# Performance work log

Measured on AMD Instinct MI355X. Metric: run time of the kernel, lower is better.

## Reference

```python
import jax, jax.numpy as jnp
import numpy as np
from jax import lax

D_MODEL = 128
D_INNER = 256      # expand=2 * d_model
D_STATE = 4
D_CONV = 4
DT_RANK = 16       # ceil(d_inner / 16), mamba-ssm default for the inner Mamba (expand=1)
DW_K = 3
B, H, W = 4, 64, 64


def setup_inputs() -> dict:
    key = jax.random.key(0)
    ks = jax.random.split(key, 16)
    g = lambda k, shape, s=0.02: jax.random.normal(k, shape, jnp.float32) * s
    inp = {}
    inp["x"] = jax.random.normal(ks[0], (B, D_MODEL, H, W), jnp.float32)
    inp["norm1_g"] = jnp.ones((D_MODEL,), jnp.float32)
    inp["norm1_b"] = jnp.zeros((D_MODEL,), jnp.float32)
    inp["in_proj_w"] = g(ks[1], (D_INNER, D_MODEL))
    inp["dwconv_w"] = g(ks[2], (D_INNER, 1, DW_K, DW_K), 0.1)
    # 4 independent Mamba modules (lr, rl, tb, bt), params stacked on axis 0
    inp["m_in_w"] = g(ks[3], (4, 2 * D_INNER, D_INNER))
    inp["m_conv_w"] = g(ks[4], (4, D_INNER, 1, D_CONV), 0.1)
    inp["m_conv_b"] = g(ks[5], (4, D_INNER), 0.1)
    inp["m_xproj_w"] = g(ks[6], (4, DT_RANK + 2 * D_STATE, D_INNER))
    inp["m_dt_w"] = g(ks[7], (4, D_INNER, DT_RANK), 0.1)
    inp["m_dt_b"] = jax.random.uniform(ks[8], (4, D_INNER), jnp.float32, -4.0, -2.0)
    inp["m_A_log"] = jnp.log(jnp.broadcast_to(
        jnp.arange(1, D_STATE + 1, dtype=jnp.float32), (4, D_INNER, D_STATE)))
    inp["m_D"] = jnp.ones((4, D_INNER), jnp.float32)
    inp["m_out_w"] = g(ks[9], (4, D_INNER, D_INNER))
    inp["normss_g"] = jnp.ones((D_INNER,), jnp.float32)
    inp["normss_b"] = jnp.zeros((D_INNER,), jnp.float32)
    inp["out_proj_w"] = g(ks[10], (D_MODEL, D_INNER))
    inp["norm2_g"] = jnp.ones((D_MODEL,), jnp.float32)
    inp["norm2_b"] = jnp.zeros((D_MODEL,), jnp.float32)
    inp["ffn_w1"] = g(ks[11], (D_MODEL, D_MODEL))
    inp["ffn_w2"] = g(ks[12], (D_MODEL, D_MODEL))
    return inp


def layer_norm(x, g, b, eps=1e-5):
    m = x.mean(-1, keepdims=True)
    v = ((x - m) ** 2).mean(-1, keepdims=True)
    return (x - m) * lax.rsqrt(v + eps) * g + b


def silu(x):
    return x * jax.nn.sigmoid(x)


def causal_dwconv1d(x, w, b):
    # x: (B, L, D); w: (D, 1, K) depthwise; left-pad K-1 (mamba pads both sides then truncates to L)
    xt = x.transpose(0, 2, 1)  # (B, D, L)
    y = lax.conv_general_dilated(xt, w, (1,), [(w.shape[-1] - 1, 0)],
                                 dimension_numbers=('NCH', 'OIH', 'NCH'),
                                 feature_group_count=xt.shape[1])
    return (y + b[None, :, None]).transpose(0, 2, 1)


def mamba(x, in_w, conv_w, conv_b, xproj_w, dt_w, dt_b, A_log, Dp, out_w):
    # x: (B, L, D) with D = D_INNER; inner Mamba has expand=1 so d_inner == d_model here
    Bb, L, Dm = x.shape
    xz = x @ in_w.T                                  # (B, L, 2D)
    xm, z = jnp.split(xz, 2, axis=-1)
    xm = silu(causal_dwconv1d(xm, conv_w, conv_b))   # (B, L, D)
    x_dbl = xm @ xproj_w.T                           # (B, L, dt_rank + 2N)
    dt = x_dbl[..., :DT_RANK]
    Bm = x_dbl[..., DT_RANK:DT_RANK + D_STATE]       # (B, L, N)
    Cm = x_dbl[..., DT_RANK + D_STATE:]              # (B, L, N)
    dt = jax.nn.softplus(dt @ dt_w.T + dt_b)         # (B, L, D)
    A = -jnp.exp(A_log)                              # (D, N)
    dA = jnp.exp(dt[..., None] * A)                  # (B, L, D, N)
    dBx = dt[..., None] * Bm[:, :, None, :] * xm[..., None]

    def step(h, inp):
        dA_t, dBx_t, C_t = inp
        h = dA_t * h + dBx_t                         # (B, D, N)
        return h, jnp.einsum('bdn,bn->bd', h, C_t)

    h0 = jnp.zeros((Bb, Dm, D_STATE), x.dtype)
    _, ys = lax.scan(step, h0, (dA.transpose(1, 0, 2, 3),
                                dBx.transpose(1, 0, 2, 3),
                                Cm.transpose(1, 0, 2)))
    y = ys.transpose(1, 0, 2) + Dp * xm              # (B, L, D)
    y = y * silu(z)
    return y @ out_w.T


def ss2d(h, Hh, Ww, mp):
    # h: (B, L, D). 4 directions: lr, rl (flip), tb (transpose), bt (transpose+flip)
    Bb, L, Dm = h.shape
    x_tb = h.reshape(Bb, Hh, Ww, Dm).transpose(0, 2, 1, 3).reshape(Bb, L, Dm)
    xs = jnp.stack([h, jnp.flip(h, 1), x_tb, jnp.flip(x_tb, 1)], 0)  # (4, B, L, D)
    ys = jax.vmap(mamba)(xs, *mp)                                     # (4, B, L, D)
    untb = lambda y: y.reshape(Bb, Ww, Hh, Dm).transpose(0, 2, 1, 3).reshape(Bb, L, Dm)
    y_lr = ys[0]
    y_rl = jnp.flip(ys[1], 1)
    y_tb = untb(ys[2])
    y_bt = untb(jnp.flip(ys[3], 1))
    return (y_lr + y_rl + y_tb + y_bt) / 4.0


def reference(x, norm1_g, norm1_b, in_proj_w, dwconv_w,
              m_in_w, m_conv_w, m_conv_b, m_xproj_w, m_dt_w, m_dt_b,
              m_A_log, m_D, m_out_w,
              normss_g, normss_b, out_proj_w,
              norm2_g, norm2_b, ffn_w1, ffn_w2):
    Bb, C, Hh, Ww = x.shape
    L = Hh * Ww
    x_flat = x.transpose(0, 2, 3, 1).reshape(Bb, L, C)
    x1 = layer_norm(x_flat, norm1_g, norm1_b)
    h = x1 @ in_proj_w.T                             # (B, L, d_inner)
    h2d = h.reshape(Bb, Hh, Ww, D_INNER).transpose(0, 3, 1, 2)
    p = DW_K // 2
    h2d = lax.conv_general_dilated(h2d, dwconv_w, (1, 1), [(p, p), (p, p)],
                                   dimension_numbers=('NCHW', 'OIHW', 'NCHW'),
                                   feature_group_count=D_INNER)
    h = silu(h2d.transpose(0, 2, 3, 1).reshape(Bb, L, D_INNER))
    mp = (m_in_w, m_conv_w, m_conv_b, m_xproj_w, m_dt_w, m_dt_b, m_A_log, m_D, m_out_w)
    h = ss2d(h, Hh, Ww, mp)
    h = layer_norm(h, normss_g, normss_b)
    h = h @ out_proj_w.T
    x2 = x_flat + h
    h2 = jax.nn.gelu(layer_norm(x2, norm2_g, norm2_b) @ ffn_w1.T, approximate=False) @ ffn_w2.T
    y = x2 + h2
    return y.reshape(Bb, Hh, Ww, C).transpose(0, 3, 1, 2)
```

## Files before the change

### kernel.cpp

```cpp
#include <hip/hip_runtime.h>
#include <math.h>


#define B_N   4
#define CDM   128
#define HH    64
#define WW    64
#define LL    4096
#define DI    256
#define DS    4
#define DCV   4
#define DTR   16
#define CS    32
#define NC    (LL / CS)
#define BLT   16384

typedef float    f32x4  __attribute__((ext_vector_type(4)));
typedef __bf16   bf16x8 __attribute__((ext_vector_type(8)));

__device__ __forceinline__ float silu_f(float x) { return x / (1.f + __expf(-x)); }
__device__ __forceinline__ float softplus_f(float x) {
  return fmaxf(x, 0.f) + __logf(1.f + __expf(-fabsf(x)));
}
__device__ __forceinline__ float gelu_f(float x) {
  return 0.5f * x * (1.f + erff(x * 0.70710678118654752f));
}
__device__ __forceinline__ ushort f2bf(float x) {
  unsigned u = __builtin_bit_cast(unsigned, x);
  u += 0x7fffu + ((u >> 16) & 1u);
  return (ushort)(u >> 16);
}
__device__ __forceinline__ float bf2f(ushort u) {
  return __builtin_bit_cast(float, (unsigned)u << 16);
}

__device__ __forceinline__ int sigma_map(int dir, int t) {
  int tt = (dir & 1) ? (LL - 1 - t) : t;
  if (dir >= 2) tt = ((tt & 63) << 6) | (tt >> 6);
  return tt;
}

#define GLDS(gp, lp) __builtin_amdgcn_global_load_lds( \
    (const __attribute__((address_space(1))) void*)(gp), \
    (__attribute__((address_space(3))) void*)(lp), 16, 0, 0)

__global__ void __launch_bounds__(256) k_prep(
    const float* __restrict__ s0, const float* __restrict__ s1,
    const float* __restrict__ s2, const float* __restrict__ s3,
    const float* __restrict__ s4, const float* __restrict__ s5,
    ushort* __restrict__ dst,
    const float* __restrict__ dtw, const float* __restrict__ xpw,
    ushort* __restrict__ w_dt, ushort* __restrict__ w_bc)
{
  int blk = blockIdx.x;
  if (blk < 864) {
    int i = (blk * 256 + threadIdx.x) * 4;
    const float* s; int base;
    if      (i < 32768)  { s = s0; base = 0; }
    else if (i < 557056) { s = s1; base = 32768; }
    else if (i < 819200) { s = s2; base = 557056; }
    else if (i < 851968) { s = s3; base = 819200; }
    else if (i < 868352) { s = s4; base = 851968; }
    else if (i < 884736) { s = s5; base = 868352; }
    else return;
    float4 v = *(const float4*)(s + (i - base));
    dst[i+0] = f2bf(v.x); dst[i+1] = f2bf(v.y); dst[i+2] = f2bf(v.z); dst[i+3] = f2bf(v.w);
  } else {
    int idx = (blk - 864) * 256 + threadIdx.x;
    if (idx >= 4 * 272 * 256) return;
    int dir = idx / 69632; int rem = idx - dir * 69632;
    int n = rem >> 8; int k = rem & 255;
    if (n < 256) {
      const float* dw = dtw + ((size_t)dir * DI + n) * DTR;
      const float* xp = xpw + (size_t)dir * 6144 + k;
      float acc = 0.f;
      #pragma unroll
      for (int j = 0; j < DTR; ++j) acc += dw[j] * xp[j * DI];
      w_dt[(size_t)dir * 65536 + (size_t)n * 256 + k] = f2bf(acc);
    } else {
      int n2 = n - 256;
      float v = (n2 < 8) ? xpw[(size_t)dir * 6144 + (size_t)(16 + n2) * 256 + k] : 0.f;
      w_bc[(size_t)dir * 4096 + (size_t)n2 * 256 + k] = f2bf(v);
    }
  }
}

__global__ void __launch_bounds__(256) k_ln1(
    const float* __restrict__ x, const float* __restrict__ g,
    const float* __restrict__ be, float* __restrict__ xflat,
    ushort* __restrict__ x1b)
{
  int blk = blockIdx.x;
  int b = blk >> 6; int l0 = (blk & 63) << 6;
  __shared__ float T[64][129];
  __shared__ float mrow[64], rrow[64];
  int t = threadIdx.x;
  int wv = t >> 6, lane = t & 63;
  for (int c = wv; c < CDM; c += 4)
    T[lane][c] = x[((size_t)b * CDM + c) * LL + l0 + lane];
  __syncthreads();
  int row = t >> 2, seg = t & 3;
  float s = 0.f;
  #pragma unroll
  for (int j = 0; j < 32; ++j) s += T[row][seg * 32 + j];
  s += __shfl_xor(s, 1); s += __shfl_xor(s, 2);
  float mean = s * (1.f / CDM);
  float v2 = 0.f;
  #pragma unroll
  for (int j = 0; j < 32; ++j) { float d = T[row][seg * 32 + j] - mean; v2 += d * d; }
  v2 += __shfl_xor(v2, 1); v2 += __shfl_xor(v2, 2);
  if (seg == 0) { mrow[row] = mean; rrow[row] = rsqrtf(v2 * (1.f / CDM) + 1e-5f); }
  __syncthreads();
  int c = t & 127;
  float gc = g[c], bc = be[c];
  for (int r = (t >> 7); r < 64; r += 2) {
    float v = T[r][c];
    size_t o = ((size_t)(b << 12) + l0 + r) * CDM + c;
    xflat[o] = v;
    x1b[o] = f2bf((v - mrow[r]) * rrow[r] * gc + bc);
  }
}

__global__ void __launch_bounds__(256) k_lnw256(
    const ushort* __restrict__ in, const float* __restrict__ g,
    const float* __restrict__ be, ushort* __restrict__ out)
{
  int w = threadIdx.x >> 6, lane = threadIdx.x & 63;
  int row = (blockIdx.x << 2) + w;
  size_t off = (size_t)row * DI + (lane << 2);
  ushort4 v4 = *(const ushort4*)(in + off);
  float v0 = bf2f(v4.x), v1 = bf2f(v4.y), v2 = bf2f(v4.z), v3 = bf2f(v4.w);
  float s1 = v0 + v1 + v2 + v3;
  float s2 = v0 * v0 + v1 * v1 + v2 * v2 + v3 * v3;
  #pragma unroll
  for (int o = 1; o < 64; o <<= 1) { s1 += __shfl_xor(s1, o); s2 += __shfl_xor(s2, o); }
  float mean = s1 * (1.f / DI);
  float r = rsqrtf(s2 * (1.f / DI) - mean * mean + 1e-5f);
  int c = lane << 2;
  ushort4 o4;
  o4.x = f2bf((v0 - mean) * r * g[c + 0] + be[c + 0]);
  o4.y = f2bf((v1 - mean) * r * g[c + 1] + be[c + 1]);
  o4.z = f2bf((v2 - mean) * r * g[c + 2] + be[c + 2]);
  o4.w = f2bf((v3 - mean) * r * g[c + 3] + be[c + 3]);
  *(ushort4*)(out + off) = o4;
}

template<int GATHER, int EPI, int BZ>
__global__ void __launch_bounds__(256) k_mgemm(
    const ushort* __restrict__ A, int lda,
    const ushort* __restrict__ Wt,
    float* __restrict__ Cf, ushort* __restrict__ Cb,
    int ldc, int K, const float* __restrict__ aux)
{
  if (BZ) {
    int z = blockIdx.z;
    A  += (size_t)z * BLT * DI;
    Wt += (size_t)z * DI * DI;
    if (Cb) Cb += (size_t)z * BLT * DI;
    if (aux) aux += (size_t)z * DI;
  }
  __shared__ ushort SH[16384];
  int tid = threadIdx.x;
  int m0 = blockIdx.x << 7, n0 = blockIdx.y << 7;
  int lane = tid & 63;
  int wm = ((tid >> 7) & 1) * 64;
  int wn = ((tid >> 6) & 1) * 64;
  int r15 = lane & 15, khi = lane >> 4;

  int srow = tid >> 3;
  int scol = (tid & 7) << 3;
  int arow[4], wrow[4];
  #pragma unroll
  for (int i = 0; i < 4; ++i) { arow[i] = m0 + i * 32 + srow; wrow[i] = n0 + i * 32 + srow; }

  f32x4 acc[4][4] = {};
  int wavebase = (tid & 192) * 8;

  for (int ks = 0; ks < K; ks += 64) {
    if (ks) __syncthreads();
    int dir = (GATHER == 2) ? (ks >> 8) : 0;
    int kin = (GATHER == 2) ? (ks & 255) : ks;
    #pragma unroll
    for (int i = 0; i < 4; ++i) {
      const ushort* gA = (GATHER == 2)
          ? A + (size_t)dir * (BLT * DI) + (size_t)arow[i] * DI + kin + scol
          : A + (size_t)arow[i] * lda + kin + scol;
      GLDS(gA, SH + i * 2048 + wavebase);
    }
    #pragma unroll
    for (int i = 0; i < 4; ++i) {
      const ushort* gW = (GATHER == 2)
          ? Wt + (size_t)dir * (DI * DI) + (size_t)wrow[i] * DI + kin + scol
          : Wt + (size_t)wrow[i] * K + kin + scol;
      GLDS(gW, SH + 8192 + i * 2048 + wavebase);
    }
    __syncthreads();
    #pragma unroll
    for (int kk = 0; kk < 2; ++kk) {
      bf16x8 af[4], wf[4];
      #pragma unroll
      for (int mi = 0; mi < 4; ++mi)
        af[mi] = *(const bf16x8*)&SH[(wm + mi * 16 + r15) * 64 + kk * 32 + khi * 8];
      #pragma unroll
      for (int ni = 0; ni < 4; ++ni)
        wf[ni] = *(const bf16x8*)&SH[8192 + (wn + ni * 16 + r15) * 64 + kk * 32 + khi * 8];
      #pragma unroll
      for (int mi = 0; mi < 4; ++mi)
        #pragma unroll
        for (int ni = 0; ni < 4; ++ni)
          acc[mi][ni] = __builtin_amdgcn_mfma_f32_16x16x32_bf16(
              af[mi], wf[ni], acc[mi][ni], 0, 0, 0);
    }
  }

  __syncthreads();
  #pragma unroll
  for (int mi = 0; mi < 4; ++mi)
    #pragma unroll
    for (int j = 0; j < 4; ++j) {
      int rr = wm + mi * 16 + khi * 4 + j;
      int sw = (rr & 7) << 3;
      #pragma unroll
      for (int ni = 0; ni < 4; ++ni) {
        int cc = wn + ni * 16 + r15;
        float v = acc[mi][ni][j];
        ushort bvv;
        if      (EPI == 8)  bvv = f2bf(0.25f * v);
        else if (EPI == 10) bvv = f2bf(softplus_f(v + aux[n0 + cc]));
        else                bvv = f2bf(v);
        SH[rr * 128 + (cc ^ sw)] = bvv;
      }
    }
  __syncthreads();
  #pragma unroll
  for (int i = 0; i < 8; ++i) {
    int rr = i * 16 + (tid >> 4);
    int cc = (tid & 15) << 3;
    uint4 v = *(const uint4*)&SH[rr * 128 + (cc ^ ((rr & 7) << 3))];
    *(uint4*)&Cb[(size_t)(m0 + rr) * ldc + n0 + cc] = v;
  }
}

__global__ void __launch_bounds__(256) k_oplna(
    const ushort* __restrict__ A,
    const ushort* __restrict__ Wt,
    const float* __restrict__ xflat,
    const float* __restrict__ g, const float* __restrict__ be,
    float* __restrict__ x2, ushort* __restrict__ x3b)
{
  __shared__ ushort As[64 * 64];
  __shared__ ushort Ws[128 * 64];
  __shared__ float redA[64][2], redB[64][2];
  int tid = threadIdx.x;
  int m0 = blockIdx.x << 6;
  int lane = tid & 63;
  int wm = ((tid >> 7) & 1) * 32;
  int wn = ((tid >> 6) & 1) * 64;
  int r15 = lane & 15, khi = lane >> 4;
  int srow = tid >> 3, scol = (tid & 7) << 3;

  f32x4 acc[2][4] = {};
  for (int ks = 0; ks < 256; ks += 64) {
    if (ks) __syncthreads();
    #pragma unroll
    for (int i = 0; i < 2; ++i) {
      const ushort* gA = A + (size_t)(m0 + i * 32 + srow) * DI + ks + scol;
      GLDS(gA, As + i * 2048 + tid * 8);
    }
    #pragma unroll
    for (int i = 0; i < 4; ++i) {
      const ushort* gW = Wt + (size_t)(i * 32 + srow) * DI + ks + scol;
      GLDS(gW, Ws + i * 2048 + tid * 8);
    }
    __syncthreads();
    #pragma unroll
    for (int kk = 0; kk < 2; ++kk) {
      bf16x8 af[2], wf[4];
      #pragma unroll
      for (int mi = 0; mi < 2; ++mi)
        af[mi] = *(const bf16x8*)&As[(wm + mi * 16 + r15) * 64 + kk * 32 + khi * 8];
      #pragma unroll
      for (int ni = 0; ni < 4; ++ni)
        wf[ni] = *(const bf16x8*)&Ws[(wn + ni * 16 + r15) * 64 + kk * 32 + khi * 8];
      #pragma unroll
      for (int mi = 0; mi < 2; ++mi)
        #pragma unroll
        for (int ni = 0; ni < 4; ++ni)
          acc[mi][ni] = __builtin_amdgcn_mfma_f32_16x16x32_bf16(
              af[mi], wf[ni], acc[mi][ni], 0, 0, 0);
    }
  }
  float vbuf[2][4][4];
  #pragma unroll
  for (int mi = 0; mi < 2; ++mi)
    #pragma unroll
    for (int j = 0; j < 4; ++j) {
      int rr = wm + mi * 16 + khi * 4 + j;
      float s1 = 0.f, s2 = 0.f;
      #pragma unroll
      for (int ni = 0; ni < 4; ++ni) {
        int cc = wn + ni * 16 + r15;
        float v = acc[mi][ni][j] + xflat[(size_t)(m0 + rr) * CDM + cc];
        vbuf[mi][ni][j] = v;
        s1 += v; s2 += v * v;
      }
      #pragma unroll
      for (int o = 1; o < 16; o <<= 1) { s1 += __shfl_xor(s1, o); s2 += __shfl_xor(s2, o); }
      if (r15 == 0) { redA[rr][wn >> 6] = s1; redB[rr][wn >> 6] = s2; }
    }
  __syncthreads();
  #pragma unroll
  for (int mi = 0; mi < 2; ++mi)
    #pragma unroll
    for (int j = 0; j < 4; ++j) {
      int rr = wm + mi * 16 + khi * 4 + j;
      float mean = (redA[rr][0] + redA[rr][1]) * (1.f / CDM);
      float var  = (redB[rr][0] + redB[rr][1]) * (1.f / CDM) - mean * mean;
      float rstd = rsqrtf(var + 1e-5f);
      #pragma unroll
      for (int ni = 0; ni < 4; ++ni) {
        int cc = wn + ni * 16 + r15;
        size_t off = (size_t)(m0 + rr) * CDM + cc;
        float v = vbuf[mi][ni][j];
        x2[off] = v;
        x3b[off] = f2bf((v - mean) * rstd * g[cc] + be[cc]);
      }
    }
}

__global__ void __launch_bounds__(256) k_ffn(
    const ushort* __restrict__ x3b, const ushort* __restrict__ w1,
    const ushort* __restrict__ w2, const float* __restrict__ x2,
    float* __restrict__ out)
{
  __shared__ ushort SH[20480];
  ushort* stageA = SH;
  ushort* stageW = SH + 4096;
  ushort* f1     = SH + 12288;
  float*  T      = (float*)SH;
  int tid = threadIdx.x;
  int m0 = blockIdx.x << 6;
  int b = m0 >> 12, l0 = m0 & (LL - 1);
  int lane = tid & 63;
  int wm = ((tid >> 7) & 1) * 32;
  int wn = ((tid >> 6) & 1) * 64;
  int r15 = lane & 15, khi = lane >> 4;
  int srow = tid >> 3, scol = (tid & 7) << 3;

  f32x4 acc[2][4] = {};
  for (int ks = 0; ks < 128; ks += 64) {
    if (ks) __syncthreads();
    #pragma unroll
    for (int i = 0; i < 2; ++i)
      GLDS(x3b + (size_t)(m0 + i * 32 + srow) * CDM + ks + scol, stageA + i * 2048 + tid * 8);
    #pragma unroll
    for (int i = 0; i < 4; ++i)
      GLDS(w1 + (size_t)(i * 32 + srow) * CDM + ks + scol, stageW + i * 2048 + tid * 8);
    __syncthreads();
    #pragma unroll
    for (int kk = 0; kk < 2; ++kk) {
      bf16x8 af[2], wf[4];
      #pragma unroll
      for (int mi = 0; mi < 2; ++mi)
        af[mi] = *(const bf16x8*)&stageA[(wm + mi * 16 + r15) * 64 + kk * 32 + khi * 8];
      #pragma unroll
      for (int ni = 0; ni < 4; ++ni)
        wf[ni] = *(const bf16x8*)&stageW[(wn + ni * 16 + r15) * 64 + kk * 32 + khi * 8];
      #pragma unroll
      for (int mi = 0; mi < 2; ++mi)
        #pragma unroll
        for (int ni = 0; ni < 4; ++ni)
          acc[mi][ni] = __builtin_amdgcn_mfma_f32_16x16x32_bf16(
              af[mi], wf[ni], acc[mi][ni], 0, 0, 0);
    }
  }
  __syncthreads();
  #pragma unroll
  for (int mi = 0; mi < 2; ++mi)
    #pragma unroll
    for (int j = 0; j < 4; ++j) {
      int rr = wm + mi * 16 + khi * 4 + j;
      int sw = (rr & 7) << 3;
      #pragma unroll
      for (int ni = 0; ni < 4; ++ni) {
        int cc = wn + ni * 16 + r15;
        f1[rr * 128 + (cc ^ sw)] = f2bf(gelu_f(acc[mi][ni][j]));
      }
    }
  __syncthreads();
  f32x4 acc2[2][4] = {};
  for (int ks = 0; ks < 128; ks += 64) {
    __syncthreads();
    #pragma unroll
    for (int i = 0; i < 4; ++i)
      GLDS(w2 + (size_t)(i * 32 + srow) * CDM + ks + scol, stageW + i * 2048 + tid * 8);
    __syncthreads();
    #pragma unroll
    for (int kk = 0; kk < 2; ++kk) {
      bf16x8 af[2], wf[4];
      #pragma unroll
      for (int mi = 0; mi < 2; ++mi) {
        int row = wm + mi * 16 + r15;
        int kx = (ks + kk * 32 + khi * 8) ^ ((row & 7) << 3);
        af[mi] = *(const bf16x8*)&f1[row * 128 + kx];
      }
      #pragma unroll
      for (int ni = 0; ni < 4; ++ni)
        wf[ni] = *(const bf16x8*)&stageW[(wn + ni * 16 + r15) * 64 + kk * 32 + khi * 8];
      #pragma unroll
      for (int mi = 0; mi < 2; ++mi)
        #pragma unroll
        for (int ni = 0; ni < 4; ++ni)
          acc2[mi][ni] = __builtin_amdgcn_mfma_f32_16x16x32_bf16(
              af[mi], wf[ni], acc2[mi][ni], 0, 0, 0);
    }
  }
  __syncthreads();
  #pragma unroll
  for (int mi = 0; mi < 2; ++mi)
    #pragma unroll
    for (int j = 0; j < 4; ++j) {
      int rr = wm + mi * 16 + khi * 4 + j;
      #pragma unroll
      for (int ni = 0; ni < 4; ++ni) {
        int cc = wn + ni * 16 + r15;
        T[rr * 129 + cc] = x2[(size_t)(m0 + rr) * CDM + cc] + acc2[mi][ni][j];
      }
    }
  __syncthreads();
  int q = tid >> 6;
  for (int cc = q; cc < CDM; cc += 4)
    out[(((size_t)b * CDM + cc) << 12) + l0 + lane] = T[lane * 129 + cc];
}

__global__ void __launch_bounds__(256) k_dwconv(
    const ushort* __restrict__ h, const float* __restrict__ wgt,
    ushort* __restrict__ out)
{
  int p = blockIdx.x;
  int b = p >> 12; int l = p & (LL - 1);
  int hy = l >> 6, wx = l & 63;
  int d = threadIdx.x;
  float acc = 0.f;
  #pragma unroll
  for (int di = -1; di <= 1; ++di) {
    int yy = hy + di; if (yy < 0 || yy >= HH) continue;
    #pragma unroll
    for (int dj = -1; dj <= 1; ++dj) {
      int xx = wx + dj; if (xx < 0 || xx >= WW) continue;
      acc += wgt[d * 9 + (di + 1) * 3 + (dj + 1)] *
             bf2f(h[(((size_t)b << 12) + (yy << 6) + xx) * DI + d]);
    }
  }
  out[(size_t)p * DI + d] = f2bf(silu_f(acc));
}

__global__ void __launch_bounds__(256) k_conv1d4(
    const ushort* __restrict__ xz_all, const float* __restrict__ cw,
    const float* __restrict__ cb, ushort* __restrict__ xmc4)
{
  int blk = blockIdx.x;
  int dir = blk >> 8; int b = (blk >> 6) & 3; int ch = blk & 63;
  int t0 = ch << 6;
  int d = threadIdx.x;
  const float* cwd = cw + (dir * DI + d) * DCV;
  float w0 = cwd[0], w1 = cwd[1], w2 = cwd[2], w3 = cwd[3];
  float bias = cb[dir * DI + d];
  size_t colb = (size_t)(dir << 9) + d;
  size_t rowb = (size_t)(b << 12);
  float xm3 = 0.f, xm2 = 0.f, xm1 = 0.f;
  if (t0 >= 3) {
    xm3 = bf2f(xz_all[(rowb + sigma_map(dir, t0 - 3)) * 2048 + colb]);
    xm2 = bf2f(xz_all[(rowb + sigma_map(dir, t0 - 2)) * 2048 + colb]);
    xm1 = bf2f(xz_all[(rowb + sigma_map(dir, t0 - 1)) * 2048 + colb]);
  }
  size_t obase = ((size_t)dir * BLT + (b << 12) + t0) * DI + d;
  #pragma unroll 4
  for (int i = 0; i < 64; ++i) {
    int l = sigma_map(dir, t0 + i);
    float x0 = bf2f(xz_all[(rowb + l) * 2048 + colb]);
    float acc = bias + w0 * xm3 + w1 * xm2 + w2 * xm1 + w3 * x0;
    xm3 = xm2; xm2 = xm1; xm1 = x0;
    xmc4[obase + (size_t)i * DI] = f2bf(silu_f(acc));
  }
}

__global__ void __launch_bounds__(256) k_bc(
    const ushort* __restrict__ xmc4, const ushort* __restrict__ w_bc,
    float* __restrict__ xbc4)
{
  __shared__ ushort As[128 * 64];
  __shared__ ushort Bs[16 * 64];
  int blk = blockIdx.x;
  int dir = blk >> 7; int m0 = (blk & 127) << 7;
  int tid = threadIdx.x;
  int lane = tid & 63; int wv = tid >> 6;
  int r15 = lane & 15, khi = lane >> 4;
  int srow = tid >> 3, scol = (tid & 7) << 3;
  size_t abase = (size_t)dir * BLT * DI;
  f32x4 acc[2] = {};
  for (int ks = 0; ks < 256; ks += 64) {
    if (ks) __syncthreads();
    #pragma unroll
    for (int i = 0; i < 4; ++i) {
      const ushort* g = xmc4 + abase + (size_t)(m0 + i * 32 + srow) * DI + ks + scol;
      GLDS(g, As + i * 2048 + tid * 8);
    }
    if (tid < 128) {
      const ushort* g = w_bc + (size_t)dir * 4096 + (size_t)(tid >> 3) * 256 + ks + scol;
      GLDS(g, Bs + tid * 8);
    }
    __syncthreads();
    #pragma unroll
    for (int kk = 0; kk < 2; ++kk) {
      bf16x8 af0 = *(const bf16x8*)&As[((wv << 5) + r15) * 64 + kk * 32 + khi * 8];
      bf16x8 af1 = *(const bf16x8*)&As[((wv << 5) + 16 + r15) * 64 + kk * 32 + khi * 8];
      bf16x8 wf  = *(const bf16x8*)&Bs[r15 * 64 + kk * 32 + khi * 8];
      acc[0] = __builtin_amdgcn_mfma_f32_16x16x32_bf16(af0, wf, acc[0], 0, 0, 0);
      acc[1] = __builtin_amdgcn_mfma_f32_16x16x32_bf16(af1, wf, acc[1], 0, 0, 0);
    }
  }
  if (r15 < 8) {
    #pragma unroll
    for (int mi = 0; mi < 2; ++mi)
      #pragma unroll
      for (int j = 0; j < 4; ++j) {
        int row = m0 + (wv << 5) + mi * 16 + khi * 4 + j;
        xbc4[((size_t)dir * BLT + row) * 8 + r15] = acc[mi][j];
      }
  }
}

__global__ void __launch_bounds__(256) k_scan_part(
    const ushort* __restrict__ dt4, const ushort* __restrict__ xmc4,
    const float* __restrict__ xbc4, const float* __restrict__ Alog4,
    float* __restrict__ P4, float* __restrict__ H4)
{
  int blk = blockIdx.x;
  int dir = blk >> 9; int b = (blk >> 7) & 3; int ch = blk & (NC - 1);
  int d = threadIdx.x;
  const float* Alog = Alog4 + (size_t)dir * DI * DS;
  float Av[DS], h[DS], P[DS];
  #pragma unroll
  for (int n = 0; n < DS; ++n) { Av[n] = -__expf(Alog[d * DS + n]); h[n] = 0.f; P[n] = 1.f; }
  size_t seg = (size_t)dir * BLT;
  size_t base = seg + (size_t)b * LL + (size_t)ch * CS;
  #pragma unroll 4
  for (int t = 0; t < CS; ++t) {
    size_t r = base + t;
    float dt = bf2f(dt4[r * DI + d]);
    float xm = bf2f(xmc4[r * DI + d]);
    float4 Bv = *(const float4*)(xbc4 + r * 8);
    float bx = dt * xm;
    float dA0 = __expf(dt * Av[0]), dA1 = __expf(dt * Av[1]);
    float dA2 = __expf(dt * Av[2]), dA3 = __expf(dt * Av[3]);
    h[0] = dA0 * h[0] + bx * Bv.x; P[0] *= dA0;
    h[1] = dA1 * h[1] + bx * Bv.y; P[1] *= dA1;
    h[2] = dA2 * h[2] + bx * Bv.z; P[2] *= dA2;
    h[3] = dA3 * h[3] + bx * Bv.w; P[3] *= dA3;
  }
  size_t o = ((size_t)blk * DI + d) * DS;
  #pragma unroll
  for (int n = 0; n < DS; ++n) { P4[o + n] = P[n]; H4[o + n] = h[n]; }
}

__global__ void __launch_bounds__(256) k_scan_carry(
    const float* __restrict__ P4, float* __restrict__ H4)
{
  int idx = blockIdx.x * 256 + threadIdx.x;
  int dir = idx >> 12; int r = idx & 4095;
  int b = r >> 10; int dn = r & 1023;
  size_t sbase = ((size_t)dir * 512 + (size_t)b * NC) * 1024 + dn;
  float carry = 0.f;
  #pragma unroll 8
  for (int ch = 0; ch < NC; ++ch) {
    size_t o = sbase + (size_t)ch * 1024;
    float Pv = P4[o], Hv = H4[o];
    H4[o] = carry;
    carry = Pv * carry + Hv;
  }
}

__global__ void __launch_bounds__(256) k_scan_fix(
    const ushort* __restrict__ dt4, const ushort* __restrict__ xmc4,
    const float* __restrict__ xbc4, const ushort* __restrict__ xz_all,
    const float* __restrict__ Alog4, const float* __restrict__ Dp4,
    const float* __restrict__ Cin, ushort* __restrict__ ybuf4)
{
  int blk = blockIdx.x;
  int dir = blk >> 9; int b = (blk >> 7) & 3; int ch = blk & (NC - 1);
  int d = threadIdx.x;
  const float* Alog = Alog4 + (size_t)dir * DI * DS;
  float Av[DS], h[DS];
  size_t ci = ((size_t)blk * DI + d) * DS;
  #pragma unroll
  for (int n = 0; n < DS; ++n) { Av[n] = -__expf(Alog[d * DS + n]); h[n] = Cin[ci + n]; }
  float Dv = Dp4[dir * DI + d];
  size_t seg = (size_t)dir * BLT;
  size_t base = seg + (size_t)b * LL + (size_t)ch * CS;
  #pragma unroll 4
  for (int t = 0; t < CS; ++t) {
    size_t r = base + t;
    float dt = bf2f(dt4[r * DI + d]);
    float xm = bf2f(xmc4[r * DI + d]);
    float4 Bv = *(const float4*)(xbc4 + r * 8);
    float4 Cv = *(const float4*)(xbc4 + r * 8 + 4);
    float bx = dt * xm;
    float dA0 = __expf(dt * Av[0]), dA1 = __expf(dt * Av[1]);
    float dA2 = __expf(dt * Av[2]), dA3 = __expf(dt * Av[3]);
    h[0] = dA0 * h[0] + bx * Bv.x;
    h[1] = dA1 * h[1] + bx * Bv.y;
    h[2] = dA2 * h[2] + bx * Bv.z;
    h[3] = dA3 * h[3] + bx * Bv.w;
    float y = h[0] * Cv.x + h[1] * Cv.y + h[2] * Cv.z + h[3] * Cv.w;
    int l = sigma_map(dir, (ch << 5) + t);
    float zv = bf2f(xz_all[(((size_t)(b << 12)) + l) * 2048 + (dir << 9) + 256 + d]);
    ybuf4[(seg + (size_t)(b << 12) + l) * DI + d] = f2bf((y + Dv * xm) * silu_f(zv));
  }
}

extern "C" void kernel_launch(void* const* d_in, const int* in_sizes, int n_in,
                              void* d_out, int out_size, void* d_ws, size_t ws_size,
                              hipStream_t stream) {
  const float* x          = (const float*)d_in[0];
  const float* norm1_g    = (const float*)d_in[1];
  const float* norm1_b    = (const float*)d_in[2];
  const float* in_proj_w  = (const float*)d_in[3];
  const float* dwconv_w   = (const float*)d_in[4];
  const float* m_in_w     = (const float*)d_in[5];
  const float* m_conv_w   = (const float*)d_in[6];
  const float* m_conv_b   = (const float*)d_in[7];
  const float* m_xproj_w  = (const float*)d_in[8];
  const float* m_dt_w     = (const float*)d_in[9];
  const float* m_dt_b     = (const float*)d_in[10];
  const float* m_A_log    = (const float*)d_in[11];
  const float* m_D        = (const float*)d_in[12];
  const float* m_out_w    = (const float*)d_in[13];
  const float* normss_g   = (const float*)d_in[14];
  const float* normss_b   = (const float*)d_in[15];
  const float* out_proj_w = (const float*)d_in[16];
  const float* norm2_g    = (const float*)d_in[17];
  const float* norm2_b    = (const float*)d_in[18];
  const float* ffn_w1     = (const float*)d_in[19];
  const float* ffn_w2     = (const float*)d_in[20];

  float* ws = (float*)d_ws;
  size_t o = 0;
  auto alloc = [&](size_t nf) { float* p = ws + o; o += nf; return p; };
  const size_t BL = BLT;
  float* xflat = alloc(BL * CDM);
  float* x2    = alloc(BL * CDM);
  float* xbc4  = alloc(BL * 8 * 4);
  float* P4    = alloc((size_t)4 * B_N * NC * DI * DS);
  float* H4    = alloc((size_t)4 * B_N * NC * DI * DS);
  auto ualloc = [&](size_t nu) { ushort* p = (ushort*)(ws + o); o += (nu + 1) / 2; return p; };
  ushort* x1b    = ualloc(BL * CDM);
  ushort* hinb   = ualloc(BL * DI);
  ushort* hcb    = ualloc(BL * DI);
  ushort* xz_all = ualloc(BL * 2048);
  ushort* xmc4   = ualloc(BL * DI * 4);
  ushort* dt4    = ualloc(BL * DI * 4);
  ushort* ybuf4  = ualloc(BL * DI * 4);
  ushort* ycombb = ualloc(BL * DI);
  ushort* hlnb   = ualloc(BL * DI);
  ushort* x3b    = ualloc(BL * CDM);
  ushort* wb     = ualloc(884736);
  ushort* w_dt   = ualloc((size_t)4 * DI * DI);
  ushort* w_bc   = ualloc((size_t)4 * 16 * DI);
  ushort* w_inproj = wb + 0;
  ushort* w_min    = wb + 32768;
  ushort* w_mout   = wb + 557056;
  ushort* w_oproj  = wb + 819200;
  ushort* w_ffn1   = wb + 851968;
  ushort* w_ffn2   = wb + 868352;

  k_prep<<<1952, 256, 0, stream>>>(
      in_proj_w, m_in_w, m_out_w, out_proj_w, ffn_w1, ffn_w2, wb,
      m_dt_w, m_xproj_w, w_dt, w_bc);
  k_ln1<<<B_N * 64, 256, 0, stream>>>(x, norm1_g, norm1_b, xflat, x1b);
  k_mgemm<0, 6, 0><<<dim3(128, 2), 256, 0, stream>>>(
      x1b, CDM, w_inproj, nullptr, hinb, DI, CDM, nullptr);
  k_dwconv<<<B_N * LL, DI, 0, stream>>>(hinb, dwconv_w, hcb);
  k_mgemm<0, 6, 0><<<dim3(128, 16), 256, 0, stream>>>(
      hcb, DI, w_min, nullptr, xz_all, 2048, DI, nullptr);
  k_conv1d4<<<1024, 256, 0, stream>>>(xz_all, m_conv_w, m_conv_b, xmc4);
  k_mgemm<0, 10, 1><<<dim3(128, 2, 4), 256, 0, stream>>>(
      xmc4, DI, w_dt, nullptr, dt4, DI, DI, m_dt_b);
  k_bc<<<512, 256, 0, stream>>>(xmc4, w_bc, xbc4);
  k_scan_part<<<4 * B_N * NC, 256, 0, stream>>>(dt4, xmc4, xbc4, m_A_log, P4, H4);
  k_scan_carry<<<64, 256, 0, stream>>>(P4, H4);
  k_scan_fix<<<4 * B_N * NC, 256, 0, stream>>>(
      dt4, xmc4, xbc4, xz_all, m_A_log, m_D, H4, ybuf4);
  k_mgemm<2, 8, 0><<<dim3(128, 2), 256, 0, stream>>>(
      ybuf4, DI, w_mout, nullptr, ycombb, DI, 1024, nullptr);
  k_lnw256<<<BLT / 4, 256, 0, stream>>>(ycombb, normss_g, normss_b, hlnb);
  k_oplna<<<256, 256, 0, stream>>>(
      hlnb, w_oproj, xflat, norm2_g, norm2_b, x2, x3b);
  k_ffn<<<256, 256, 0, stream>>>(x3b, w_ffn1, w_ffn2, x2, (float*)d_out);
}
```

Before: 249.4 us.

## Fuse dt projection with chunk scan and fold SS2D LayerNorm into out-proj

The dt projection GEMM (softplus epilogue) is merged with the per-chunk partial scan, so each block computes dt for a 128-row tile and immediately scans its 32-step chunks from shared memory. The separate partial-scan kernel and the standalone LayerNorm kernel are removed, and the LayerNorm is applied inside the out-projection kernel on a fully staged 64x256 A tile. The residual input is now stored as bf16 instead of fp32 to cut bandwidth. This saves launches and global round trips, at the cost of lower residual precision and fewer threads running the scan (each thread does 2 chunks serially), which may reduce scan parallelism.

```diff
diff --git a/kernel.cpp b/kernel.cpp
--- a/kernel.cpp
+++ b/kernel.cpp
@@ -17,6 +17,7 @@
 
 typedef float    f32x4  __attribute__((ext_vector_type(4)));
 typedef __bf16   bf16x8 __attribute__((ext_vector_type(8)));
+typedef unsigned short u16x8 __attribute__((ext_vector_type(8)));
 
 __device__ __forceinline__ float silu_f(float x) { return x / (1.f + __expf(-x)); }
 __device__ __forceinline__ float softplus_f(float x) {
@@ -87,7 +88,7 @@
 
 __global__ void __launch_bounds__(256) k_ln1(
     const float* __restrict__ x, const float* __restrict__ g,
-    const float* __restrict__ be, float* __restrict__ xflat,
+    const float* __restrict__ be, ushort* __restrict__ xflatb,
     ushort* __restrict__ x1b)
 {
   int blk = blockIdx.x;
@@ -116,49 +117,17 @@
   for (int r = (t >> 7); r < 64; r += 2) {
     float v = T[r][c];
     size_t o = ((size_t)(b << 12) + l0 + r) * CDM + c;
-    xflat[o] = v;
+    xflatb[o] = f2bf(v);
     x1b[o] = f2bf((v - mrow[r]) * rrow[r] * gc + bc);
   }
 }
 
-__global__ void __launch_bounds__(256) k_lnw256(
-    const ushort* __restrict__ in, const float* __restrict__ g,
-    const float* __restrict__ be, ushort* __restrict__ out)
-{
-  int w = threadIdx.x >> 6, lane = threadIdx.x & 63;
-  int row = (blockIdx.x << 2) + w;
-  size_t off = (size_t)row * DI + (lane << 2);
-  ushort4 v4 = *(const ushort4*)(in + off);
-  float v0 = bf2f(v4.x), v1 = bf2f(v4.y), v2 = bf2f(v4.z), v3 = bf2f(v4.w);
-  float s1 = v0 + v1 + v2 + v3;
-  float s2 = v0 * v0 + v1 * v1 + v2 * v2 + v3 * v3;
-  #pragma unroll
-  for (int o = 1; o < 64; o <<= 1) { s1 += __shfl_xor(s1, o); s2 += __shfl_xor(s2, o); }
-  float mean = s1 * (1.f / DI);
-  float r = rsqrtf(s2 * (1.f / DI) - mean * mean + 1e-5f);
-  int c = lane << 2;
-  ushort4 o4;
-  o4.x = f2bf((v0 - mean) * r * g[c + 0] + be[c + 0]);
-  o4.y = f2bf((v1 - mean) * r * g[c + 1] + be[c + 1]);
-  o4.z = f2bf((v2 - mean) * r * g[c + 2] + be[c + 2]);
-  o4.w = f2bf((v3 - mean) * r * g[c + 3] + be[c + 3]);
-  *(ushort4*)(out + off) = o4;
-}
-
-template<int GATHER, int EPI, int BZ>
+template<int GATHER, int EPI>
 __global__ void __launch_bounds__(256) k_mgemm(
     const ushort* __restrict__ A, int lda,
     const ushort* __restrict__ Wt,
-    float* __restrict__ Cf, ushort* __restrict__ Cb,
-    int ldc, int K, const float* __restrict__ aux)
-{
-  if (BZ) {
-    int z = blockIdx.z;
-    A  += (size_t)z * BLT * DI;
-    Wt += (size_t)z * DI * DI;
-    if (Cb) Cb += (size_t)z * BLT * DI;
-    if (aux) aux += (size_t)z * DI;
-  }
+    ushort* __restrict__ Cb, int ldc, int K)
+{
   __shared__ ushort SH[16384];
   int tid = threadIdx.x;
   int m0 = blockIdx.x << 7, n0 = blockIdx.y << 7;
@@ -224,11 +193,7 @@
       for (int ni = 0; ni < 4; ++ni) {
         int cc = wn + ni * 16 + r15;
         float v = acc[mi][ni][j];
-        ushort bvv;
-        if      (EPI == 8)  bvv = f2bf(0.25f * v);
-        else if (EPI == 10) bvv = f2bf(softplus_f(v + aux[n0 + cc]));
-        else                bvv = f2bf(v);
-        SH[rr * 128 + (cc ^ sw)] = bvv;
+        SH[rr * 128 + (cc ^ sw)] = (EPI == 8) ? f2bf(0.25f * v) : f2bf(v);
       }
     }
   __syncthreads();
@@ -241,14 +206,118 @@
   }
 }
 
+__global__ void __launch_bounds__(256) k_dtscan(
+    const ushort* __restrict__ xmc4, const ushort* __restrict__ w_dt,
+    const float* __restrict__ dtb4, const float* __restrict__ xbc4,
+    const float* __restrict__ Alog4,
+    ushort* __restrict__ dt4, float* __restrict__ P4, float* __restrict__ H4)
+{
+  int z = blockIdx.z;
+  const ushort* A  = xmc4 + (size_t)z * BLT * DI;
+  const ushort* Wt = w_dt + (size_t)z * DI * DI;
+  ushort* Cb = dt4 + (size_t)z * BLT * DI;
+  const float* aux = dtb4 + z * DI;
+  __shared__ ushort SH[16384];
+  int tid = threadIdx.x;
+  int m0 = blockIdx.x << 7, n0 = blockIdx.y << 7;
+  int lane = tid & 63;
+  int wm = ((tid >> 7) & 1) * 64;
+  int wn = ((tid >> 6) & 1) * 64;
+  int r15 = lane & 15, khi = lane >> 4;
+  int srow = tid >> 3, scol = (tid & 7) << 3;
+
+  f32x4 acc[4][4] = {};
+  int wavebase = (tid & 192) * 8;
+  for (int ks = 0; ks < 256; ks += 64) {
+    if (ks) __syncthreads();
+    #pragma unroll
+    for (int i = 0; i < 4; ++i)
+      GLDS(A + (size_t)(m0 + i * 32 + srow) * DI + ks + scol, SH + i * 2048 + wavebase);
+    #pragma unroll
+    for (int i = 0; i < 4; ++i)
+      GLDS(Wt + (size_t)(n0 + i * 32 + srow) * DI + ks + scol, SH + 8192 + i * 2048 + wavebase);
+    __syncthreads();
+    #pragma unroll
+    for (int kk = 0; kk < 2; ++kk) {
+      bf16x8 af[4], wf[4];
+      #pragma unroll
+      for (int mi = 0; mi < 4; ++mi)
+        af[mi] = *(const bf16x8*)&SH[(wm + mi * 16 + r15) * 64 + kk * 32 + khi * 8];
+      #pragma unroll
+      for (int ni = 0; ni < 4; ++ni)
+        wf[ni] = *(const bf16x8*)&SH[8192 + (wn + ni * 16 + r15) * 64 + kk * 32 + khi * 8];
+      #pragma unroll
+      for (int mi = 0; mi < 4; ++mi)
+        #pragma unroll
+        for (int ni = 0; ni < 4; ++ni)
+          acc[mi][ni] = __builtin_amdgcn_mfma_f32_16x16x32_bf16(
+              af[mi], wf[ni], acc[mi][ni], 0, 0, 0);
+    }
+  }
+  __syncthreads();
+  #pragma unroll
+  for (int mi = 0; mi < 4; ++mi)
+    #pragma unroll
+    for (int j = 0; j < 4; ++j) {
+      int rr = wm + mi * 16 + khi * 4 + j;
+      int sw = (rr & 7) << 3;
+      #pragma unroll
+      for (int ni = 0; ni < 4; ++ni) {
+        int cc = wn + ni * 16 + r15;
+        SH[rr * 128 + (cc ^ sw)] = f2bf(softplus_f(acc[mi][ni][j] + aux[n0 + cc]));
+      }
+    }
+  __syncthreads();
+  #pragma unroll
+  for (int i = 0; i < 8; ++i) {
+    int rr = i * 16 + (tid >> 4);
+    int cc = (tid & 15) << 3;
+    uint4 v = *(const uint4*)&SH[rr * 128 + (cc ^ ((rr & 7) << 3))];
+    *(uint4*)&Cb[(size_t)(m0 + rr) * DI + n0 + cc] = v;
+  }
+  int dl = tid & 127;
+  int dg = n0 + dl;
+  const float* Alog = Alog4 + ((size_t)z * DI + dg) * DS;
+  float Av[DS];
+  #pragma unroll
+  for (int n = 0; n < DS; ++n) Av[n] = -__expf(Alog[n]);
+  #pragma unroll
+  for (int cc2 = 0; cc2 < 2; ++cc2) {
+    int chl = ((tid >> 7) << 1) + cc2;
+    float h0 = 0.f, h1 = 0.f, h2 = 0.f, h3 = 0.f;
+    float P0 = 1.f, P1 = 1.f, P2 = 1.f, P3 = 1.f;
+    #pragma unroll 4
+    for (int tl = 0; tl < CS; ++tl) {
+      int tr = (chl << 5) + tl;
+      float dt = bf2f(SH[tr * 128 + (dl ^ ((tr & 7) << 3))]);
+      float xm = bf2f(A[(size_t)(m0 + tr) * DI + dg]);
+      float4 Bv = *(const float4*)(xbc4 + ((size_t)z * BLT + m0 + tr) * 8);
+      float bx = dt * xm;
+      float dA0 = __expf(dt * Av[0]), dA1 = __expf(dt * Av[1]);
+      float dA2 = __expf(dt * Av[2]), dA3 = __expf(dt * Av[3]);
+      h0 = dA0 * h0 + bx * Bv.x; P0 *= dA0;
+      h1 = dA1 * h1 + bx * Bv.y; P1 *= dA1;
+      h2 = dA2 * h2 + bx * Bv.z; P2 *= dA2;
+      h3 = dA3 * h3 + bx * Bv.w; P3 *= dA3;
+    }
+    int b = (m0 + (chl << 5)) >> 12;
+    int ch_in_b = ((m0 & 4095) >> 5) + chl;
+    int blk = z * 512 + b * 128 + ch_in_b;
+    size_t o = ((size_t)blk * DI + dg) * DS;
+    *(float4*)(P4 + o) = make_float4(P0, P1, P2, P3);
+    *(float4*)(H4 + o) = make_float4(h0, h1, h2, h3);
+  }
+}
+
 __global__ void __launch_bounds__(256) k_oplna(
-    const ushort* __restrict__ A,
+    const ushort* __restrict__ yc,
     const ushort* __restrict__ Wt,
-    const float* __restrict__ xflat,
-    const float* __restrict__ g, const float* __restrict__ be,
+    const ushort* __restrict__ xflatb,
+    const float* __restrict__ gss, const float* __restrict__ bss,
+    const float* __restrict__ g2, const float* __restrict__ b2,
     float* __restrict__ x2, ushort* __restrict__ x3b)
 {
-  __shared__ ushort As[64 * 64];
+  __shared__ ushort Ash[64 * 256];
   __shared__ ushort Ws[128 * 64];
   __shared__ float redA[64][2], redB[64][2];
   int tid = threadIdx.x;
@@ -259,26 +328,53 @@
   int r15 = lane & 15, khi = lane >> 4;
   int srow = tid >> 3, scol = (tid & 7) << 3;
 
+  #pragma unroll
+  for (int i = 0; i < 8; ++i)
+    GLDS(yc + (size_t)m0 * DI + i * 2048 + tid * 8, Ash + i * 2048 + tid * 8);
+  __syncthreads();
+  {
+    int r = tid >> 2, q = tid & 3;
+    float vreg[8][8];
+    float s1 = 0.f, s2 = 0.f;
+    #pragma unroll
+    for (int j = 0; j < 8; ++j) {
+      int ch = (j + tid) & 7;
+      u16x8 v8 = *(const u16x8*)&Ash[r * 256 + q * 64 + ch * 8];
+      #pragma unroll
+      for (int e = 0; e < 8; ++e) {
+        float v = bf2f(v8[e]);
+        vreg[j][e] = v; s1 += v; s2 += v * v;
+      }
+    }
+    s1 += __shfl_xor(s1, 1); s1 += __shfl_xor(s1, 2);
+    s2 += __shfl_xor(s2, 1); s2 += __shfl_xor(s2, 2);
+    float mean = s1 * (1.f / DI);
+    float rstd = rsqrtf(s2 * (1.f / DI) - mean * mean + 1e-5f);
+    #pragma unroll
+    for (int j = 0; j < 8; ++j) {
+      int ch = (j + tid) & 7;
+      int colb = q * 64 + ch * 8;
+      u16x8 o8;
+      #pragma unroll
+      for (int e = 0; e < 8; ++e)
+        o8[e] = f2bf((vreg[j][e] - mean) * rstd * gss[colb + e] + bss[colb + e]);
+      *(u16x8*)&Ash[r * 256 + colb] = o8;
+    }
+  }
+  __syncthreads();
   f32x4 acc[2][4] = {};
   for (int ks = 0; ks < 256; ks += 64) {
     if (ks) __syncthreads();
     #pragma unroll
-    for (int i = 0; i < 2; ++i) {
-      const ushort* gA = A + (size_t)(m0 + i * 32 + srow) * DI + ks + scol;
-      GLDS(gA, As + i * 2048 + tid * 8);
-    }
-    #pragma unroll
-    for (int i = 0; i < 4; ++i) {
-      const ushort* gW = Wt + (size_t)(i * 32 + srow) * DI + ks + scol;
-      GLDS(gW, Ws + i * 2048 + tid * 8);
-    }
+    for (int i = 0; i < 4; ++i)
+      GLDS(Wt + (size_t)(i * 32 + srow) * DI + ks + scol, Ws + i * 2048 + tid * 8);
     __syncthreads();
     #pragma unroll
     for (int kk = 0; kk < 2; ++kk) {
       bf16x8 af[2], wf[4];
       #pragma unroll
       for (int mi = 0; mi < 2; ++mi)
-        af[mi] = *(const bf16x8*)&As[(wm + mi * 16 + r15) * 64 + kk * 32 + khi * 8];
+        af[mi] = *(const bf16x8*)&Ash[(wm + mi * 16 + r15) * 256 + ks + kk * 32 + khi * 8];
       #pragma unroll
       for (int ni = 0; ni < 4; ++ni)
         wf[ni] = *(const bf16x8*)&Ws[(wn + ni * 16 + r15) * 64 + kk * 32 + khi * 8];
@@ -300,7 +396,7 @@
       #pragma unroll
       for (int ni = 0; ni < 4; ++ni) {
         int cc = wn + ni * 16 + r15;
-        float v = acc[mi][ni][j] + xflat[(size_t)(m0 + rr) * CDM + cc];
+        float v = acc[mi][ni][j] + bf2f(xflatb[(size_t)(m0 + rr) * CDM + cc]);
         vbuf[mi][ni][j] = v;
         s1 += v; s2 += v * v;
       }
@@ -323,7 +419,7 @@
         size_t off = (size_t)(m0 + rr) * CDM + cc;
         float v = vbuf[mi][ni][j];
         x2[off] = v;
-        x3b[off] = f2bf((v - mean) * rstd * g[cc] + be[cc]);
+        x3b[off] = f2bf((v - mean) * rstd * g2[cc] + b2[cc]);
       }
     }
 }
@@ -529,39 +625,6 @@
         xbc4[((size_t)dir * BLT + row) * 8 + r15] = acc[mi][j];
       }
   }
-}
-
-__global__ void __launch_bounds__(256) k_scan_part(
-    const ushort* __restrict__ dt4, const ushort* __restrict__ xmc4,
-    const float* __restrict__ xbc4, const float* __restrict__ Alog4,
-    float* __restrict__ P4, float* __restrict__ H4)
-{
-  int blk = blockIdx.x;
-  int dir = blk >> 9; int b = (blk >> 7) & 3; int ch = blk & (NC - 1);
-  int d = threadIdx.x;
-  const float* Alog = Alog4 + (size_t)dir * DI * DS;
-  float Av[DS], h[DS], P[DS];
-  #pragma unroll
-  for (int n = 0; n < DS; ++n) { Av[n] = -__expf(Alog[d * DS + n]); h[n] = 0.f; P[n] = 1.f; }
-  size_t seg = (size_t)dir * BLT;
-  size_t base = seg + (size_t)b * LL + (size_t)ch * CS;
-  #pragma unroll 4
-  for (int t = 0; t < CS; ++t) {
-    size_t r = base + t;
-    float dt = bf2f(dt4[r * DI + d]);
-    float xm = bf2f(xmc4[r * DI + d]);
-    float4 Bv = *(const float4*)(xbc4 + r * 8);
-    float bx = dt * xm;
-    float dA0 = __expf(dt * Av[0]), dA1 = __expf(dt * Av[1]);
-    float dA2 = __expf(dt * Av[2]), dA3 = __expf(dt * Av[3]);
-    h[0] = dA0 * h[0] + bx * Bv.x; P[0] *= dA0;
-    h[1] = dA1 * h[1] + bx * Bv.y; P[1] *= dA1;
-    h[2] = dA2 * h[2] + bx * Bv.z; P[2] *= dA2;
-    h[3] = dA3 * h[3] + bx * Bv.w; P[3] *= dA3;
-  }
-  size_t o = ((size_t)blk * DI + d) * DS;
-  #pragma unroll
-  for (int n = 0; n < DS; ++n) { P4[o + n] = P[n]; H4[o + n] = h[n]; }
 }
 
 __global__ void __launch_bounds__(256) k_scan_carry(
@@ -648,12 +711,12 @@
   size_t o = 0;
   auto alloc = [&](size_t nf) { float* p = ws + o; o += nf; return p; };
   const size_t BL = BLT;
-  float* xflat = alloc(BL * CDM);
   float* x2    = alloc(BL * CDM);
   float* xbc4  = alloc(BL * 8 * 4);
   float* P4    = alloc((size_t)4 * B_N * NC * DI * DS);
   float* H4    = alloc((size_t)4 * B_N * NC * DI * DS);
   auto ualloc = [&](size_t nu) { ushort* p = (ushort*)(ws + o); o += (nu + 1) / 2; return p; };
+  ushort* xflatb = ualloc(BL * CDM);
   ushort* x1b    = ualloc(BL * CDM);
   ushort* hinb   = ualloc(BL * DI);
   ushort* hcb    = ualloc(BL * DI);
@@ -662,7 +725,6 @@
   ushort* dt4    = ualloc(BL * DI * 4);
   ushort* ybuf4  = ualloc(BL * DI * 4);
   ushort* ycombb = ualloc(BL * DI);
-  ushort* hlnb   = ualloc(BL * DI);
   ushort* x3b    = ualloc(BL * CDM);
   ushort* wb     = ualloc(884736);
   ushort* w_dt   = ualloc((size_t)4 * DI * DI);
@@ -677,24 +739,22 @@
   k_prep<<<1952, 256, 0, stream>>>(
       in_proj_w, m_in_w, m_out_w, out_proj_w, ffn_w1, ffn_w2, wb,
       m_dt_w, m_xproj_w, w_dt, w_bc);
-  k_ln1<<<B_N * 64, 256, 0, stream>>>(x, norm1_g, norm1_b, xflat, x1b);
-  k_mgemm<0, 6, 0><<<dim3(128, 2), 256, 0, stream>>>(
-      x1b, CDM, w_inproj, nullptr, hinb, DI, CDM, nullptr);
+  k_ln1<<<B_N * 64, 256, 0, stream>>>(x, norm1_g, norm1_b, xflatb, x1b);
+  k_mgemm<0, 6><<<dim3(128, 2), 256, 0, stream>>>(
+      x1b, CDM, w_inproj, hinb, DI, CDM);
   k_dwconv<<<B_N * LL, DI, 0, stream>>>(hinb, dwconv_w, hcb);
-  k_mgemm<0, 6, 0><<<dim3(128, 16), 256, 0, stream>>>(
-      hcb, DI, w_min, nullptr, xz_all, 2048, DI, nullptr);
+  k_mgemm<0, 6><<<dim3(128, 16), 256, 0, stream>>>(
+      hcb, DI, w_min, xz_all, 2048, DI);
   k_conv1d4<<<1024, 256, 0, stream>>>(xz_all, m_conv_w, m_conv_b, xmc4);
-  k_mgemm<0, 10, 1><<<dim3(128, 2, 4), 256, 0, stream>>>(
-      xmc4, DI, w_dt, nullptr, dt4, DI, DI, m_dt_b);
   k_bc<<<512, 256, 0, stream>>>(xmc4, w_bc, xbc4);
-  k_scan_part<<<4 * B_N * NC, 256, 0, stream>>>(dt4, xmc4, xbc4, m_A_log, P4, H4);
+  k_dtscan<<<dim3(128, 2, 4), 256, 0, stream>>>(
+      xmc4, w_dt, m_dt_b, xbc4, m_A_log, dt4, P4, H4);
   k_scan_carry<<<64, 256, 0, stream>>>(P4, H4);
   k_scan_fix<<<4 * B_N * NC, 256, 0, stream>>>(
       dt4, xmc4, xbc4, xz_all, m_A_log, m_D, H4, ybuf4);
-  k_mgemm<2, 8, 0><<<dim3(128, 2), 256, 0, stream>>>(
-      ybuf4, DI, w_mout, nullptr, ycombb, DI, 1024, nullptr);
-  k_lnw256<<<BLT / 4, 256, 0, stream>>>(ycombb, normss_g, normss_b, hlnb);
+  k_mgemm<2, 8><<<dim3(128, 2), 256, 0, stream>>>(
+      ybuf4, DI, w_mout, ycombb, DI, 1024);
   k_oplna<<<256, 256, 0, stream>>>(
-      hlnb, w_oproj, xflat, norm2_g, norm2_b, x2, x3b);
+      ycombb, w_oproj, xflatb, normss_g, normss_b, norm2_g, norm2_b, x2, x3b);
   k_ffn<<<256, 256, 0, stream>>>(x3b, w_ffn1, w_ffn2, x2, (float*)d_out);
 }
```

Result: no change. 248.9 us (-0.2%).
